# Performance work log

Hardware: AMD Instinct MI355X
Metric: run time of the kernel (lower is better)

The kernel has to match this reference:

```python
import jax, jax.numpy as jnp
import numpy as np

B, N, K, D = 8, 4096, 8, 256
EPS = 1e-8
LN_EPS = 1e-5


def setup_inputs() -> dict:
    key = jax.random.key(0)
    ks = jax.random.split(key, 9)
    lim_s = float(np.sqrt(6.0 / (K + D)))   # xavier_uniform on (K, D) fan dims
    lim_w = float(np.sqrt(6.0 / (D + D)))   # xavier-ish init for square Linear weights
    return {
        "embeddings": jax.random.normal(ks[0], (B, N, D), jnp.float32),
        "slots_mu": jax.random.uniform(ks[1], (1, K, D), jnp.float32, -lim_s, lim_s),
        "slots_logsigma": jax.random.uniform(ks[2], (1, K, D), jnp.float32, -lim_s, lim_s),
        "mixing_coeffs": jnp.full((1, K), 1.0 / K, jnp.float32),
        "Wq": jax.random.uniform(ks[3], (D, D), jnp.float32, -lim_w, lim_w),
        "Wk": jax.random.uniform(ks[4], (D, D), jnp.float32, -lim_w, lim_w),
        "Wv": jax.random.uniform(ks[5], (D, D), jnp.float32, -lim_w, lim_w),
        "ln_scale": jnp.ones((D,), jnp.float32),
        "ln_bias": jnp.zeros((D,), jnp.float32),
        "noise_init": jax.random.normal(ks[6], (B, K, D), jnp.float32),
        "noise_final": jax.random.normal(ks[7], (B, K, D), jnp.float32),
        "num_iterations": 3,
    }


def _layer_norm(x, scale, bias):
    m = jnp.mean(x, axis=-1, keepdims=True)
    v = jnp.mean((x - m) ** 2, axis=-1, keepdims=True)  # biased var, matches torch LayerNorm
    return (x - m) / jnp.sqrt(v + LN_EPS) * scale + bias


def reference(embeddings, slots_mu, slots_logsigma, mixing_coeffs, Wq, Wk, Wv,
              ln_scale, ln_bias, noise_init, noise_final, num_iterations):
    b, n, d = embeddings.shape
    k = slots_mu.shape[1]
    mix = jnp.broadcast_to(mixing_coeffs, (b, k))               # (B,K)
    mu = jnp.broadcast_to(slots_mu, (b, k, d))                  # (B,K,D)
    sigma = jnp.exp(jnp.broadcast_to(slots_logsigma, (b, k, d)))
    slots = mu + sigma * noise_init                             # slots never updated in loop (faithful)

    x = _layer_norm(embeddings, ln_scale, ln_bias)
    keys = x @ Wk.T                                             # (B,N,D)
    values = x @ Wv.T                                           # (B,N,D)

    log_norm_const = jnp.float32(-0.5 * d * np.log(2.0 * np.pi))
    attn = None
    for _ in range(num_iterations):
        queries = slots @ Wq.T                                  # (B,K,D)
        diff = keys[:, :, None, :] - queries[:, None, :, :]     # (B,N,K,D)
        gll = -0.5 * jnp.sum(diff ** 2 / (sigma[:, None] ** 2 + EPS), axis=-1)  # (B,N,K)
        gll = (log_norm_const
               - 0.5 * jnp.sum(jnp.log(jnp.abs(sigma) + EPS), axis=-1)[:, None, :]
               + gll)
        gll = jnp.clip(gll, -10000.0, 10000.0)
        log_attn = jnp.log(mix + EPS)[:, None, :] + gll         # (B,N,K)
        attn = jax.nn.softmax(log_attn, axis=1)                 # softmax over N
        mu = jnp.einsum('bnk,bnd->bkd', attn, values)           # weighted mean
        diff_v = values[:, :, None, :] - mu[:, None, :, :]      # (B,N,K,D)
        sigma = jnp.einsum('bnk,bnkd->bkd', attn, diff_v ** 2)  # weighted variance
        mix = jnp.sum(attn, axis=1) / n

    sigma = jnp.maximum(jnp.abs(sigma), EPS)
    slots_out = mu + sigma * noise_final
    return slots_out, jnp.transpose(attn, (0, 2, 1))            # (B,K,D), (B,K,N)
```

## Files before the change

### kernel.cpp

```cpp
#include <hip/hip_runtime.h>
#include <math.h>


#define Bd 8
#define Nd 4096
#define Kd 8
#define Dd 256
#define Md (Bd*Nd)
#define NITER 3
#define EPSf 1e-8f
#define LNEPS 1e-5f
#define NCH 64
#define LOGNORM -235.24826450039617f

typedef float f32x4 __attribute__((ext_vector_type(4)));
typedef short bf16x8 __attribute__((ext_vector_type(8)));
typedef unsigned short ushort_t;
typedef unsigned short us4 __attribute__((ext_vector_type(4)));

#define KEYS_OFF 0
#define VALS_OFF (Md*Dd)
#define E_OFF    (2*Md*Dd)
#define Q_OFF    (E_OFF + Bd*Kd*Nd)
#define W_OFF    (Q_OFF + Bd*Kd*Dd)
#define CST_OFF  (W_OFF + Bd*Kd*Dd)
#define MSP_OFF  (CST_OFF + 64)
#define SSP_OFF  (MSP_OFF + Bd*Kd*NCH)
#define PMU_OFF  (SSP_OFF + Bd*Kd*NCH)
#define PS2_OFF  (PMU_OFF + Bd*NCH*Kd*Dd)
#define WH_OFF   (PS2_OFF + Bd*NCH*Kd*Dd)
#define WL_OFF   (WH_OFF + 65536)
#define XH_OFF   (WL_OFF + 65536)
#define XL_OFF   (XH_OFF + Md*Dd/2)
#define WS_TOTAL (XL_OFF + Md*Dd/2)

__device__ __forceinline__ ushort_t f2bf(float f) {
    unsigned u = __float_as_uint(f);
    return (ushort_t)((u + 0x7FFFu + ((u >> 16) & 1u)) >> 16);
}
__device__ __forceinline__ float b2f(ushort_t h) {
    return __uint_as_float(((unsigned)h) << 16);
}
__device__ __forceinline__ void gload_lds16(const void* g, void* l) {
    __builtin_amdgcn_global_load_lds(
        (__attribute__((address_space(1))) void*)g,
        (__attribute__((address_space(3))) void*)l, 16, 0, 0);
}

__global__ __launch_bounds__(256) void k_setup(
        const float* __restrict__ emb, const float* __restrict__ lns,
        const float* __restrict__ lnb, const float* __restrict__ Wk,
        const float* __restrict__ Wv, const float* __restrict__ mu0,
        const float* __restrict__ lsig, const float* __restrict__ nz0,
        const float* __restrict__ Wq, ushort_t* __restrict__ xh,
        ushort_t* __restrict__ xl, ushort_t* __restrict__ Wh,
        ushort_t* __restrict__ Wl, float* __restrict__ qout,
        float* __restrict__ w_ws, float* __restrict__ cst_ws) {
    __shared__ float s_s[256];
    __shared__ float red[256];
    const int bx = blockIdx.x;
    if (bx < 1024) {
        const int tid = threadIdx.x, wave = tid >> 6, lane = tid & 63;
        const int row0 = bx * 32;
        const float4 sc = ((const float4*)lns)[lane];
        const float4 bi = ((const float4*)lnb)[lane];
        for (int rr = 0; rr < 8; ++rr) {
            const int r = row0 + wave * 8 + rr;
            const float4 e4 = ((const float4*)(emb + (size_t)r * Dd))[lane];
            float s = e4.x + e4.y + e4.z + e4.w;
            #pragma unroll
            for (int off = 32; off; off >>= 1) s += __shfl_xor(s, off);
            const float m = s * (1.0f / 256.0f);
            const float dx = e4.x - m, dy = e4.y - m, dz = e4.z - m, dw = e4.w - m;
            float ss = dx * dx + dy * dy + dz * dz + dw * dw;
            #pragma unroll
            for (int off = 32; off; off >>= 1) ss += __shfl_xor(ss, off);
            const float rs = 1.0f / sqrtf(ss * (1.0f / 256.0f) + LNEPS);
            float x[4];
            x[0] = dx * rs * sc.x + bi.x;
            x[1] = dy * rs * sc.y + bi.y;
            x[2] = dz * rs * sc.z + bi.z;
            x[3] = dw * rs * sc.w + bi.w;
            us4 h4, l4;
            #pragma unroll
            for (int j = 0; j < 4; ++j) {
                const ushort_t h = f2bf(x[j]);
                h4[j] = h;
                l4[j] = f2bf(x[j] - b2f(h));
            }
            *(us4*)(xh + (size_t)r * Dd + lane * 4) = h4;
            *(us4*)(xl + (size_t)r * Dd + lane * 4) = l4;
        }
    } else if (bx < 1536) {
        const int r = bx - 1024, d = threadIdx.x;
        const float w = (r < 256) ? Wk[(size_t)r * 256 + d]
                                  : Wv[(size_t)(r - 256) * 256 + d];
        const ushort_t h = f2bf(w);
        Wh[(size_t)r * 256 + d] = h;
        Wl[(size_t)r * 256 + d] = f2bf(w - b2f(h));
    } else {
        const int bk = bx - 1536;
        const int k = bk & 7;
        const int d = threadIdx.x;
        const float sg = expf(lsig[k * 256 + d]);
        s_s[d] = mu0[k * 256 + d] + sg * nz0[(size_t)bk * 256 + d];
        w_ws[(size_t)bk * 256 + d] = 1.0f / (sg * sg + EPSf);
        red[d] = logf(fabsf(sg) + EPSf);
        __syncthreads();
        for (int s = 128; s; s >>= 1) {
            if (d < s) red[d] += red[d + s];
            __syncthreads();
        }
        if (d == 0) cst_ws[bk] = LOGNORM - 0.5f * red[0];
        float acc = 0.0f;
        const float4* Wr = (const float4*)(Wq + (size_t)d * 256);
        const float4* sp = (const float4*)s_s;
        #pragma unroll 8
        for (int j = 0; j < 64; ++j) {
            const float4 w4 = Wr[j], s4 = sp[j];
            acc += w4.x * s4.x + w4.y * s4.y + w4.z * s4.z + w4.w * s4.w;
        }
        qout[(size_t)bk * 256 + d] = acc;
    }
}

__global__ __launch_bounds__(256, 2) void k_gemm(
        const ushort_t* __restrict__ xh, const ushort_t* __restrict__ xl,
        const ushort_t* __restrict__ Wh, const ushort_t* __restrict__ Wl,
        float* __restrict__ keys, float* __restrict__ vals) {
    __shared__ ushort_t Ah[128 * 32], Al[128 * 32];
    __shared__ ushort_t Bh[256 * 32], Bl[256 * 32];
    const int bxf = blockIdx.x;
    const int grp = bxf >> 4, o = bxf & 15;
    const int tile = grp * 8 + (o & 7);
    const int cb = o >> 3;
    const int tid = threadIdx.x, lane = tid & 63, wave = tid >> 6;
    const int row0 = tile * 128;
    const int wm = wave >> 1, wn = wave & 1;

    f32x4 acc[4][8];
    #pragma unroll
    for (int a = 0; a < 4; ++a)
        #pragma unroll
        for (int b = 0; b < 8; ++b) acc[a][b] = (f32x4)(0.0f);

    for (int jb = 0; jb < 256; jb += 32) {
        #pragma unroll
        for (int i = 0; i < 2; ++i) {
            const int p = tid + i * 256;
            const int r = p >> 2, gp = p & 3;
            const int g = gp ^ ((r >> 1) & 3);
            const size_t goff = (size_t)(row0 + r) * 256 + jb + g * 8;
            gload_lds16(xh + goff, &Ah[p * 8]);
            gload_lds16(xl + goff, &Al[p * 8]);
        }
        #pragma unroll
        for (int i = 0; i < 4; ++i) {
            const int p = (wave * 4 + i) * 64 + lane;
            const int r = p >> 2, gp = p & 3;
            const int g = gp ^ ((r >> 1) & 3);
            const size_t goff = (size_t)(cb * 256 + r) * 256 + jb + g * 8;
            gload_lds16(Wh + goff, &Bh[p * 8]);
            gload_lds16(Wl + goff, &Bl[p * 8]);
        }
        __syncthreads();

        bf16x8 bhf[8], blf[8];
        #pragma unroll
        for (int ni = 0; ni < 8; ++ni) {
            const int c = wn * 128 + ni * 16 + (lane & 15);
            const int g = lane >> 4;
            const int off = c * 32 + ((g ^ ((c >> 1) & 3)) << 3);
            bhf[ni] = *(const bf16x8*)&Bh[off];
            blf[ni] = *(const bf16x8*)&Bl[off];
        }
        #pragma unroll
        for (int mi = 0; mi < 4; ++mi) {
            const int rr = wm * 64 + mi * 16 + (lane & 15);
            const int g = lane >> 4;
            const int off = rr * 32 + ((g ^ ((rr >> 1) & 3)) << 3);
            const bf16x8 ah = *(const bf16x8*)&Ah[off];
            const bf16x8 al = *(const bf16x8*)&Al[off];
            #pragma unroll
            for (int ni = 0; ni < 8; ++ni) {
                acc[mi][ni] = __builtin_amdgcn_mfma_f32_16x16x32_bf16(ah, bhf[ni], acc[mi][ni], 0, 0, 0);
                acc[mi][ni] = __builtin_amdgcn_mfma_f32_16x16x32_bf16(ah, blf[ni], acc[mi][ni], 0, 0, 0);
                acc[mi][ni] = __builtin_amdgcn_mfma_f32_16x16x32_bf16(al, bhf[ni], acc[mi][ni], 0, 0, 0);
            }
        }
        __syncthreads();
    }
    float* outp = (cb == 0) ? keys : vals;
    #pragma unroll
    for (int mi = 0; mi < 4; ++mi) {
        const int rbase = row0 + wm * 64 + mi * 16 + ((lane >> 4) << 2);
        #pragma unroll
        for (int ni = 0; ni < 8; ++ni) {
            const int col = wn * 128 + ni * 16 + (lane & 15);
            #pragma unroll
            for (int rg = 0; rg < 4; ++rg)
                outp[(size_t)(rbase + rg) * Dd + col] = acc[mi][ni][rg];
        }
    }
}

__global__ __launch_bounds__(512, 4) void k_fuse(
        const float* __restrict__ keys, const float* __restrict__ vals,
        const float* __restrict__ q_ws, const float* __restrict__ w_ws,
        const float* __restrict__ cst_ws, float* __restrict__ e_glob,
        float* __restrict__ msp, float* __restrict__ ssp,
        float* __restrict__ pmu, float* __restrict__ ps2, const int last) {
    __shared__ float buf[16384];
    __shared__ float e_s[8][64];
    const int tid = threadIdx.x, lane = tid & 63, wv = tid >> 6;
    const int b = blockIdx.x >> 6, chunk = blockIdx.x & 63;
    const int n0 = chunk * 64;
    const int wvu = __builtin_amdgcn_readfirstlane(wv);

    const float* kbase = keys + ((size_t)b * Nd + n0) * Dd;
    #pragma unroll
    for (int i = 0; i < 8; ++i) {
        const int p = i * 512 + tid;
        const int row = p >> 6, gp = p & 63;
        const int g = gp ^ row;
        gload_lds16(kbase + (size_t)row * Dd + g * 4, &buf[p * 4]);
    }
    __syncthreads();

    const float4* qk = (const float4*)(q_ws + ((size_t)b * Kd + wvu) * Dd);
    const float4* wk = (const float4*)(w_ws + ((size_t)b * Kd + wvu) * Dd);
    const float* krow = &buf[lane * 256];
    float ax = 0.f, ay = 0.f, az = 0.f, aw = 0.f;
    #pragma unroll 8
    for (int g = 0; g < 64; ++g) {
        const float4 k4 = *(const float4*)&krow[(g ^ lane) * 4];
        const float4 q4 = qk[g];
        const float4 w4 = wk[g];
        float t;
        t = k4.x - q4.x; ax += t * t * w4.x;
        t = k4.y - q4.y; ay += t * t * w4.y;
        t = k4.z - q4.z; az += t * t * w4.z;
        t = k4.w - q4.w; aw += t * t * w4.w;
    }
    float gv = cst_ws[b * Kd + wvu] - 0.5f * ((ax + ay) + (az + aw));
    gv = fminf(fmaxf(gv, -10000.0f), 10000.0f);
    float m = gv;
    #pragma unroll
    for (int off = 32; off; off >>= 1) m = fmaxf(m, __shfl_xor(m, off));
    const float e = expf(gv - m);
    float ssum = e;
    #pragma unroll
    for (int off = 32; off; off >>= 1) ssum += __shfl_xor(ssum, off);
    e_s[wv][lane] = e;
    if (last) e_glob[((size_t)(b * Kd + wvu)) * Nd + n0 + lane] = e;
    if (lane == 0) {
        msp[(b * Kd + wvu) * NCH + chunk] = m;
        ssp[(b * Kd + wvu) * NCH + chunk] = ssum;
    }
    __syncthreads();

    const float* vbase = vals + ((size_t)b * Nd + n0) * Dd;
    #pragma unroll
    for (int i = 0; i < 8; ++i) {
        const int p = i * 512 + tid;
        gload_lds16(vbase + (size_t)p * 4, &buf[p * 4]);
    }
    __syncthreads();

    float4 mu4 = {0.f, 0.f, 0.f, 0.f}, s24 = {0.f, 0.f, 0.f, 0.f};
    #pragma unroll 8
    for (int n = 0; n < 64; ++n) {
        const float4 v = *(const float4*)&buf[n * 256 + lane * 4];
        const float a = e_s[wv][n];
        mu4.x += a * v.x; mu4.y += a * v.y; mu4.z += a * v.z; mu4.w += a * v.w;
        s24.x += a * v.x * v.x; s24.y += a * v.y * v.y;
        s24.z += a * v.z * v.z; s24.w += a * v.w * v.w;
    }
    const size_t o = (((size_t)(b * NCH + chunk)) * Kd + wv) * Dd + lane * 4;
    *(float4*)(pmu + o) = mu4;
    *(float4*)(ps2 + o) = s24;
}

__global__ __launch_bounds__(256) void k_prep(
        const float* __restrict__ msp, const float* __restrict__ ssp,
        const float* __restrict__ pmu, const float* __restrict__ ps2,
        float* __restrict__ w_ws, float* __restrict__ cst_ws,
        const float* __restrict__ nzf, float* __restrict__ slots_out,
        const float* __restrict__ e_glob, float* __restrict__ attn,
        const int last) {
    __shared__ float wS[64];
    __shared__ float aS[64];
    __shared__ float sinv_s;
    __shared__ float4 muP[4][64];
    __shared__ float4 s2P[4][64];
    const int bk = blockIdx.x;
    const int b = bk >> 3, k = bk & 7;
    const int tid = threadIdx.x, lane = tid & 63, grp = tid >> 6;
    if (grp == 0) {
        const float m_c = msp[bk * NCH + lane];
        const float s_c = ssp[bk * NCH + lane];
        float M = m_c;
        #pragma unroll
        for (int off = 32; off; off >>= 1) M = fmaxf(M, __shfl_xor(M, off));
        const float wc = expf(m_c - M);
        float S = wc * s_c;
        #pragma unroll
        for (int off = 32; off; off >>= 1) S += __shfl_xor(S, off);
        wS[lane] = wc;
        aS[lane] = wc / S;
        if (lane == 0) sinv_s = 1.0f / S;
    }
    __syncthreads();
    float4 am = {0.f, 0.f, 0.f, 0.f}, a2 = {0.f, 0.f, 0.f, 0.f};
    #pragma unroll
    for (int i = 0; i < 16; ++i) {
        const int c = grp * 16 + i;
        const float wc = wS[c];
        const size_t o = (((size_t)(b * NCH + c)) * Kd + k) * Dd + lane * 4;
        const float4 pm = *(const float4*)(pmu + o);
        const float4 p2 = *(const float4*)(ps2 + o);
        am.x += wc * pm.x; am.y += wc * pm.y; am.z += wc * pm.z; am.w += wc * pm.w;
        a2.x += wc * p2.x; a2.y += wc * p2.y; a2.z += wc * p2.z; a2.w += wc * p2.w;
    }
    muP[grp][lane] = am;
    s2P[grp][lane] = a2;
    __syncthreads();
    if (grp == 0) {
        const float sinv = sinv_s;
        float4 mu, E2;
        mu.x = (muP[0][lane].x + muP[1][lane].x + muP[2][lane].x + muP[3][lane].x) * sinv;
        mu.y = (muP[0][lane].y + muP[1][lane].y + muP[2][lane].y + muP[3][lane].y) * sinv;
        mu.z = (muP[0][lane].z + muP[1][lane].z + muP[2][lane].z + muP[3][lane].z) * sinv;
        mu.w = (muP[0][lane].w + muP[1][lane].w + muP[2][lane].w + muP[3][lane].w) * sinv;
        E2.x = (s2P[0][lane].x + s2P[1][lane].x + s2P[2][lane].x + s2P[3][lane].x) * sinv;
        E2.y = (s2P[0][lane].y + s2P[1][lane].y + s2P[2][lane].y + s2P[3][lane].y) * sinv;
        E2.z = (s2P[0][lane].z + s2P[1][lane].z + s2P[2][lane].z + s2P[3][lane].z) * sinv;
        E2.w = (s2P[0][lane].w + s2P[1][lane].w + s2P[2][lane].w + s2P[3][lane].w) * sinv;
        float4 sg;
        sg.x = E2.x - mu.x * mu.x; sg.y = E2.y - mu.y * mu.y;
        sg.z = E2.z - mu.z * mu.z; sg.w = E2.w - mu.w * mu.w;
        float4 wout;
        wout.x = 1.0f / (sg.x * sg.x + EPSf); wout.y = 1.0f / (sg.y * sg.y + EPSf);
        wout.z = 1.0f / (sg.z * sg.z + EPSf); wout.w = 1.0f / (sg.w * sg.w + EPSf);
        *(float4*)(w_ws + (size_t)bk * Dd + lane * 4) = wout;
        const float4 nz = *(const float4*)(nzf + (size_t)bk * Dd + lane * 4);
        float4 so;
        so.x = mu.x + fmaxf(fabsf(sg.x), EPSf) * nz.x;
        so.y = mu.y + fmaxf(fabsf(sg.y), EPSf) * nz.y;
        so.z = mu.z + fmaxf(fabsf(sg.z), EPSf) * nz.z;
        so.w = mu.w + fmaxf(fabsf(sg.w), EPSf) * nz.w;
        *(float4*)(slots_out + (size_t)bk * Dd + lane * 4) = so;
        float lsum = logf(fabsf(sg.x) + EPSf) + logf(fabsf(sg.y) + EPSf)
                   + logf(fabsf(sg.z) + EPSf) + logf(fabsf(sg.w) + EPSf);
        #pragma unroll
        for (int off = 32; off; off >>= 1) lsum += __shfl_xor(lsum, off);
        if (lane == 0) cst_ws[bk] = LOGNORM - 0.5f * lsum;
    }
    if (last) {
        const float4* erow = (const float4*)(e_glob + (size_t)bk * Nd);
        float4* arow = (float4*)(attn + (size_t)bk * Nd);
        #pragma unroll
        for (int i = 0; i < 4; ++i) {
            const int idx = tid + i * 256;
            const float4 e4 = erow[idx];
            const float a = aS[idx >> 4];
            float4 o4;
            o4.x = e4.x * a; o4.y = e4.y * a; o4.z = e4.z * a; o4.w = e4.w * a;
            arow[idx] = o4;
        }
    }
}

extern "C" void kernel_launch(void* const* d_in, const int* in_sizes, int n_in,
                              void* d_out, int out_size, void* d_ws, size_t ws_size,
                              hipStream_t stream) {
    const float* emb  = (const float*)d_in[0];
    const float* mu0  = (const float*)d_in[1];
    const float* lsig = (const float*)d_in[2];
    const float* Wq   = (const float*)d_in[4];
    const float* Wk   = (const float*)d_in[5];
    const float* Wv   = (const float*)d_in[6];
    const float* lns  = (const float*)d_in[7];
    const float* lnb  = (const float*)d_in[8];
    const float* nz0  = (const float*)d_in[9];
    const float* nzf  = (const float*)d_in[10];

    float* ws    = (float*)d_ws;
    float* out   = (float*)d_out;
    float* keys  = ws + KEYS_OFF;
    float* vals  = ws + VALS_OFF;
    float* eglob = ws + E_OFF;
    float* qws   = ws + Q_OFF;
    float* wws   = ws + W_OFF;
    float* cstw  = ws + CST_OFF;
    float* msp   = ws + MSP_OFF;
    float* ssp   = ws + SSP_OFF;
    float* pmu   = ws + PMU_OFF;
    float* ps2   = ws + PS2_OFF;
    ushort_t* Whp = (ushort_t*)(ws + WH_OFF);
    ushort_t* Wlp = (ushort_t*)(ws + WL_OFF);
    ushort_t* xhp = (ushort_t*)(ws + XH_OFF);
    ushort_t* xlp = (ushort_t*)(ws + XL_OFF);
    float* attn = out + Bd * Kd * Dd;

    k_setup<<<1600, 256, 0, stream>>>(emb, lns, lnb, Wk, Wv, mu0, lsig, nz0,
                                      Wq, xhp, xlp, Whp, Wlp, qws, wws, cstw);
    k_gemm<<<512, 256, 0, stream>>>(xhp, xlp, Whp, Wlp, keys, vals);
    for (int it = 0; it < NITER; ++it) {
        const int last = (it == NITER - 1);
        k_fuse<<<512, 512, 0, stream>>>(keys, vals, qws, wws, cstw, eglob,
                                        msp, ssp, pmu, ps2, last);
        k_prep<<<64, 256, 0, stream>>>(msp, ssp, pmu, ps2, wws, cstw, nzf,
                                       out, eglob, attn, last);
    }
    (void)in_sizes; (void)n_in; (void)out_size; (void)ws_size;
}
```

Before: 206.0 us.

## Split fuse kernel into 32-row chunks with 256-thread blocks, two slots per wave

Halves the N-chunk per block in the fused E-step/M-step kernel (64 to 32 rows) and uses 256-thread blocks, doubling the grid to 1024 blocks. Each wave now covers two slots, one per 32-lane half, in the log-likelihood phase and accumulates two slots' partial moments in the weighted-sum phase. The reduction kernel is updated to merge 128 chunk partials through a two-wave cross-wave max/sum. The aim is better occupancy and load balance from a larger grid with less LDS per block. The cost is twice as much partial-sum traffic written and then read back in k_prep.

```diff
diff --git a/kernel.cpp b/kernel.cpp
--- a/kernel.cpp
+++ b/kernel.cpp
@@ -10,7 +10,7 @@
 #define NITER 3
 #define EPSf 1e-8f
 #define LNEPS 1e-5f
-#define NCH 64
+#define NCH 128
 #define LOGNORM -235.24826450039617f
 
 typedef float f32x4 __attribute__((ext_vector_type(4)));
@@ -204,36 +204,38 @@
     }
 }
 
-__global__ __launch_bounds__(512, 4) void k_fuse(
+__global__ __launch_bounds__(256, 4) void k_fuse(
         const float* __restrict__ keys, const float* __restrict__ vals,
         const float* __restrict__ q_ws, const float* __restrict__ w_ws,
         const float* __restrict__ cst_ws, float* __restrict__ e_glob,
         float* __restrict__ msp, float* __restrict__ ssp,
         float* __restrict__ pmu, float* __restrict__ ps2, const int last) {
-    __shared__ float buf[16384];
-    __shared__ float e_s[8][64];
+    __shared__ float buf[8192];
+    __shared__ float e_s[8][32];
     const int tid = threadIdx.x, lane = tid & 63, wv = tid >> 6;
-    const int b = blockIdx.x >> 6, chunk = blockIdx.x & 63;
-    const int n0 = chunk * 64;
-    const int wvu = __builtin_amdgcn_readfirstlane(wv);
+    const int b = blockIdx.x >> 7, chunk = blockIdx.x & 127;
+    const int n0 = chunk * 32;
 
     const float* kbase = keys + ((size_t)b * Nd + n0) * Dd;
     #pragma unroll
     for (int i = 0; i < 8; ++i) {
-        const int p = i * 512 + tid;
+        const int p = i * 256 + tid;
         const int row = p >> 6, gp = p & 63;
         const int g = gp ^ row;
         gload_lds16(kbase + (size_t)row * Dd + g * 4, &buf[p * 4]);
     }
     __syncthreads();
 
-    const float4* qk = (const float4*)(q_ws + ((size_t)b * Kd + wvu) * Dd);
-    const float4* wk = (const float4*)(w_ws + ((size_t)b * Kd + wvu) * Dd);
-    const float* krow = &buf[lane * 256];
+    const int half = lane >> 5, nl = lane & 31;
+    const int k = wv + 4 * half;
+    const int bkf = b * Kd + k;
+    const float4* qk = (const float4*)(q_ws + (size_t)bkf * Dd);
+    const float4* wk = (const float4*)(w_ws + (size_t)bkf * Dd);
+    const float* krow = &buf[nl * 256];
     float ax = 0.f, ay = 0.f, az = 0.f, aw = 0.f;
     #pragma unroll 8
     for (int g = 0; g < 64; ++g) {
-        const float4 k4 = *(const float4*)&krow[(g ^ lane) * 4];
+        const float4 k4 = *(const float4*)&krow[((g ^ nl) & 63) * 4];
         const float4 q4 = qk[g];
         const float4 w4 = wk[g];
         float t;
@@ -242,43 +244,52 @@
         t = k4.z - q4.z; az += t * t * w4.z;
         t = k4.w - q4.w; aw += t * t * w4.w;
     }
-    float gv = cst_ws[b * Kd + wvu] - 0.5f * ((ax + ay) + (az + aw));
+    float gv = cst_ws[bkf] - 0.5f * ((ax + ay) + (az + aw));
     gv = fminf(fmaxf(gv, -10000.0f), 10000.0f);
     float m = gv;
     #pragma unroll
-    for (int off = 32; off; off >>= 1) m = fmaxf(m, __shfl_xor(m, off));
+    for (int off = 16; off; off >>= 1) m = fmaxf(m, __shfl_xor(m, off));
     const float e = expf(gv - m);
     float ssum = e;
     #pragma unroll
-    for (int off = 32; off; off >>= 1) ssum += __shfl_xor(ssum, off);
-    e_s[wv][lane] = e;
-    if (last) e_glob[((size_t)(b * Kd + wvu)) * Nd + n0 + lane] = e;
-    if (lane == 0) {
-        msp[(b * Kd + wvu) * NCH + chunk] = m;
-        ssp[(b * Kd + wvu) * NCH + chunk] = ssum;
+    for (int off = 16; off; off >>= 1) ssum += __shfl_xor(ssum, off);
+    e_s[k][nl] = e;
+    if (last) e_glob[(size_t)bkf * Nd + n0 + nl] = e;
+    if (nl == 0) {
+        msp[bkf * NCH + chunk] = m;
+        ssp[bkf * NCH + chunk] = ssum;
     }
     __syncthreads();
 
     const float* vbase = vals + ((size_t)b * Nd + n0) * Dd;
     #pragma unroll
     for (int i = 0; i < 8; ++i) {
-        const int p = i * 512 + tid;
+        const int p = i * 256 + tid;
         gload_lds16(vbase + (size_t)p * 4, &buf[p * 4]);
     }
     __syncthreads();
 
-    float4 mu4 = {0.f, 0.f, 0.f, 0.f}, s24 = {0.f, 0.f, 0.f, 0.f};
+    const int k1 = wv + 4;
+    float4 muA = {0.f,0.f,0.f,0.f}, s2A = {0.f,0.f,0.f,0.f};
+    float4 muB = {0.f,0.f,0.f,0.f}, s2B = {0.f,0.f,0.f,0.f};
     #pragma unroll 8
-    for (int n = 0; n < 64; ++n) {
+    for (int n = 0; n < 32; ++n) {
         const float4 v = *(const float4*)&buf[n * 256 + lane * 4];
-        const float a = e_s[wv][n];
-        mu4.x += a * v.x; mu4.y += a * v.y; mu4.z += a * v.z; mu4.w += a * v.w;
-        s24.x += a * v.x * v.x; s24.y += a * v.y * v.y;
-        s24.z += a * v.z * v.z; s24.w += a * v.w * v.w;
-    }
-    const size_t o = (((size_t)(b * NCH + chunk)) * Kd + wv) * Dd + lane * 4;
-    *(float4*)(pmu + o) = mu4;
-    *(float4*)(ps2 + o) = s24;
+        const float a0 = e_s[wv][n];
+        const float a1 = e_s[k1][n];
+        const float vx2 = v.x * v.x, vy2 = v.y * v.y;
+        const float vz2 = v.z * v.z, vw2 = v.w * v.w;
+        muA.x += a0 * v.x; muA.y += a0 * v.y; muA.z += a0 * v.z; muA.w += a0 * v.w;
+        s2A.x += a0 * vx2; s2A.y += a0 * vy2; s2A.z += a0 * vz2; s2A.w += a0 * vw2;
+        muB.x += a1 * v.x; muB.y += a1 * v.y; muB.z += a1 * v.z; muB.w += a1 * v.w;
+        s2B.x += a1 * vx2; s2B.y += a1 * vy2; s2B.z += a1 * vz2; s2B.w += a1 * vw2;
+    }
+    const size_t o0 = (((size_t)(b * NCH + chunk)) * Kd + wv) * Dd + lane * 4;
+    const size_t o1 = (((size_t)(b * NCH + chunk)) * Kd + k1) * Dd + lane * 4;
+    *(float4*)(pmu + o0) = muA;
+    *(float4*)(ps2 + o0) = s2A;
+    *(float4*)(pmu + o1) = muB;
+    *(float4*)(ps2 + o1) = s2B;
 }
 
 __global__ __launch_bounds__(256) void k_prep(
@@ -288,33 +299,43 @@
         const float* __restrict__ nzf, float* __restrict__ slots_out,
         const float* __restrict__ e_glob, float* __restrict__ attn,
         const int last) {
-    __shared__ float wS[64];
-    __shared__ float aS[64];
+    __shared__ float wS[128];
+    __shared__ float aS[128];
+    __shared__ float wred[2], wsum[2];
     __shared__ float sinv_s;
     __shared__ float4 muP[4][64];
     __shared__ float4 s2P[4][64];
     const int bk = blockIdx.x;
     const int b = bk >> 3, k = bk & 7;
     const int tid = threadIdx.x, lane = tid & 63, grp = tid >> 6;
-    if (grp == 0) {
-        const float m_c = msp[bk * NCH + lane];
-        const float s_c = ssp[bk * NCH + lane];
-        float M = m_c;
-        #pragma unroll
-        for (int off = 32; off; off >>= 1) M = fmaxf(M, __shfl_xor(M, off));
+    float m_c = 0.0f, s_c = 0.0f;
+    if (tid < 128) {
+        m_c = msp[bk * NCH + tid];
+        s_c = ssp[bk * NCH + tid];
+        float mm = m_c;
+        #pragma unroll
+        for (int off = 32; off; off >>= 1) mm = fmaxf(mm, __shfl_xor(mm, off));
+        if (lane == 0) wred[grp] = mm;
+    }
+    __syncthreads();
+    const float M = fmaxf(wred[0], wred[1]);
+    if (tid < 128) {
         const float wc = expf(m_c - M);
-        float S = wc * s_c;
-        #pragma unroll
-        for (int off = 32; off; off >>= 1) S += __shfl_xor(S, off);
-        wS[lane] = wc;
-        aS[lane] = wc / S;
-        if (lane == 0) sinv_s = 1.0f / S;
-    }
+        wS[tid] = wc;
+        float s = wc * s_c;
+        #pragma unroll
+        for (int off = 32; off; off >>= 1) s += __shfl_xor(s, off);
+        if (lane == 0) wsum[grp] = s;
+    }
+    __syncthreads();
+    const float S = wsum[0] + wsum[1];
+    if (tid < 128) aS[tid] = wS[tid] / S;
+    if (tid == 0) sinv_s = 1.0f / S;
     __syncthreads();
     float4 am = {0.f, 0.f, 0.f, 0.f}, a2 = {0.f, 0.f, 0.f, 0.f};
     #pragma unroll
-    for (int i = 0; i < 16; ++i) {
-        const int c = grp * 16 + i;
+    for (int i = 0; i < 32; ++i) {
+        const int c = grp * 32 + i;
         const float wc = wS[c];
         const size_t o = (((size_t)(b * NCH + c)) * Kd + k) * Dd + lane * 4;
         const float4 pm = *(const float4*)(pmu + o);
@@ -363,7 +384,7 @@
         for (int i = 0; i < 4; ++i) {
             const int idx = tid + i * 256;
             const float4 e4 = erow[idx];
-            const float a = aS[idx >> 4];
+            const float a = aS[idx >> 3];
             float4 o4;
             o4.x = e4.x * a; o4.y = e4.y * a; o4.z = e4.z * a; o4.w = e4.w * a;
             arow[idx] = o4;
@@ -408,8 +429,8 @@
     k_gemm<<<512, 256, 0, stream>>>(xhp, xlp, Whp, Wlp, keys, vals);
     for (int it = 0; it < NITER; ++it) {
         const int last = (it == NITER - 1);
-        k_fuse<<<512, 512, 0, stream>>>(keys, vals, qws, wws, cstw, eglob,
-                                        msp, ssp, pmu, ps2, last);
+        k_fuse<<<1024, 256, 0, stream>>>(keys, vals, qws, wws, cstw, eglob,
+                                         msp, ssp, pmu, ps2, last);
         k_prep<<<64, 256, 0, stream>>>(msp, ssp, pmu, ps2, wws, cstw, nzf,
                                        out, eglob, attn, last);
     }
```

After: 239.7 us. 1.16x slower.

## Double k_fuse chunk size to 128 rows with 1024-thread blocks

Applied to the files above, without the earlier changes.

k_fuse now handles 128 sequence rows per block with 16 waves, two waves per slot, and merges their max, sum and weighted moments through shared memory. The number of chunk partials drops from 64 to 32, which halves the partial buffers k_prep has to read and reduce. In exchange each block needs 128KB of LDS and extra barriers, and only 256 blocks are launched, so occupancy and latency hiding may suffer.

```diff
diff --git a/kernel.cpp b/kernel.cpp
--- a/kernel.cpp
+++ b/kernel.cpp
@@ -10,7 +10,7 @@
 #define NITER 3
 #define EPSf 1e-8f
 #define LNEPS 1e-5f
-#define NCH 64
+#define NCH 32
 #define LOGNORM -235.24826450039617f
 
 typedef float f32x4 __attribute__((ext_vector_type(4)));
@@ -204,32 +204,36 @@
     }
 }
 
-__global__ __launch_bounds__(512, 4) void k_fuse(
+__global__ __launch_bounds__(1024, 4) void k_fuse(
         const float* __restrict__ keys, const float* __restrict__ vals,
         const float* __restrict__ q_ws, const float* __restrict__ w_ws,
         const float* __restrict__ cst_ws, float* __restrict__ e_glob,
         float* __restrict__ msp, float* __restrict__ ssp,
         float* __restrict__ pmu, float* __restrict__ ps2, const int last) {
-    __shared__ float buf[16384];
-    __shared__ float e_s[8][64];
+    __shared__ float buf[32768];
+    __shared__ float e_s[8][128];
+    __shared__ float mex[8][2], sex[8][2];
     const int tid = threadIdx.x, lane = tid & 63, wv = tid >> 6;
-    const int b = blockIdx.x >> 6, chunk = blockIdx.x & 63;
-    const int n0 = chunk * 64;
-    const int wvu = __builtin_amdgcn_readfirstlane(wv);
+    const int b = blockIdx.x >> 5, chunk = blockIdx.x & 31;
+    const int n0 = chunk * 128;
+    const int k = __builtin_amdgcn_readfirstlane(wv & 7);
+    const int sub = __builtin_amdgcn_readfirstlane(wv >> 3);
+    const int bkf = b * Kd + k;
 
     const float* kbase = keys + ((size_t)b * Nd + n0) * Dd;
     #pragma unroll
     for (int i = 0; i < 8; ++i) {
-        const int p = i * 512 + tid;
-        const int row = p >> 6, gp = p & 63;
+        const int p = i * 1024 + tid;
+        const int sb = p >> 12, q = p & 4095;
+        const int row = q >> 6, gp = q & 63;
         const int g = gp ^ row;
-        gload_lds16(kbase + (size_t)row * Dd + g * 4, &buf[p * 4]);
-    }
-    __syncthreads();
-
-    const float4* qk = (const float4*)(q_ws + ((size_t)b * Kd + wvu) * Dd);
-    const float4* wk = (const float4*)(w_ws + ((size_t)b * Kd + wvu) * Dd);
-    const float* krow = &buf[lane * 256];
+        gload_lds16(kbase + (size_t)(sb * 64 + row) * Dd + g * 4, &buf[p * 4]);
+    }
+    __syncthreads();
+
+    const float4* qk = (const float4*)(q_ws + (size_t)bkf * Dd);
+    const float4* wk = (const float4*)(w_ws + (size_t)bkf * Dd);
+    const float* krow = &buf[sub * 16384 + lane * 256];
     float ax = 0.f, ay = 0.f, az = 0.f, aw = 0.f;
     #pragma unroll 8
     for (int g = 0; g < 64; ++g) {
@@ -242,27 +246,31 @@
         t = k4.z - q4.z; az += t * t * w4.z;
         t = k4.w - q4.w; aw += t * t * w4.w;
     }
-    float gv = cst_ws[b * Kd + wvu] - 0.5f * ((ax + ay) + (az + aw));
+    float gv = cst_ws[bkf] - 0.5f * ((ax + ay) + (az + aw));
     gv = fminf(fmaxf(gv, -10000.0f), 10000.0f);
     float m = gv;
     #pragma unroll
     for (int off = 32; off; off >>= 1) m = fmaxf(m, __shfl_xor(m, off));
-    const float e = expf(gv - m);
+    if (lane == 0) mex[k][sub] = m;
+    __syncthreads();
+    const float mf = fmaxf(mex[k][0], mex[k][1]);
+    const float e = expf(gv - mf);
     float ssum = e;
     #pragma unroll
     for (int off = 32; off; off >>= 1) ssum += __shfl_xor(ssum, off);
-    e_s[wv][lane] = e;
-    if (last) e_glob[((size_t)(b * Kd + wvu)) * Nd + n0 + lane] = e;
-    if (lane == 0) {
-        msp[(b * Kd + wvu) * NCH + chunk] = m;
-        ssp[(b * Kd + wvu) * NCH + chunk] = ssum;
-    }
-    __syncthreads();
+    e_s[k][sub * 64 + lane] = e;
+    if (last) e_glob[(size_t)bkf * Nd + n0 + sub * 64 + lane] = e;
+    if (lane == 0) sex[k][sub] = ssum;
+    __syncthreads();
+    if (sub == 0 && lane == 0) {
+        msp[bkf * NCH + chunk] = mf;
+        ssp[bkf * NCH + chunk] = sex[k][0] + sex[k][1];
+    }
 
     const float* vbase = vals + ((size_t)b * Nd + n0) * Dd;
     #pragma unroll
     for (int i = 0; i < 8; ++i) {
-        const int p = i * 512 + tid;
+        const int p = i * 1024 + tid;
         gload_lds16(vbase + (size_t)p * 4, &buf[p * 4]);
     }
     __syncthreads();
@@ -270,15 +278,29 @@
     float4 mu4 = {0.f, 0.f, 0.f, 0.f}, s24 = {0.f, 0.f, 0.f, 0.f};
     #pragma unroll 8
     for (int n = 0; n < 64; ++n) {
-        const float4 v = *(const float4*)&buf[n * 256 + lane * 4];
-        const float a = e_s[wv][n];
+        const int r = sub * 64 + n;
+        const float4 v = *(const float4*)&buf[r * 256 + lane * 4];
+        const float a = e_s[k][r];
         mu4.x += a * v.x; mu4.y += a * v.y; mu4.z += a * v.z; mu4.w += a * v.w;
         s24.x += a * v.x * v.x; s24.y += a * v.y * v.y;
         s24.z += a * v.z * v.z; s24.w += a * v.w * v.w;
     }
-    const size_t o = (((size_t)(b * NCH + chunk)) * Kd + wv) * Dd + lane * 4;
-    *(float4*)(pmu + o) = mu4;
-    *(float4*)(ps2 + o) = s24;
+    __syncthreads();
+    if (sub == 1) {
+        float4* scr = (float4*)&buf[k * 1024 + lane * 8];
+        scr[0] = mu4;
+        scr[1] = s24;
+    }
+    __syncthreads();
+    if (sub == 0) {
+        const float4* scr = (const float4*)&buf[k * 1024 + lane * 8];
+        const float4 pm = scr[0], p2 = scr[1];
+        mu4.x += pm.x; mu4.y += pm.y; mu4.z += pm.z; mu4.w += pm.w;
+        s24.x += p2.x; s24.y += p2.y; s24.z += p2.z; s24.w += p2.w;
+        const size_t o = (((size_t)(b * NCH + chunk)) * Kd + k) * Dd + lane * 4;
+        *(float4*)(pmu + o) = mu4;
+        *(float4*)(ps2 + o) = s24;
+    }
 }
 
 __global__ __launch_bounds__(256) void k_prep(
@@ -288,8 +310,8 @@
         const float* __restrict__ nzf, float* __restrict__ slots_out,
         const float* __restrict__ e_glob, float* __restrict__ attn,
         const int last) {
-    __shared__ float wS[64];
-    __shared__ float aS[64];
+    __shared__ float wS[32];
+    __shared__ float aS[32];
     __shared__ float sinv_s;
     __shared__ float4 muP[4][64];
     __shared__ float4 s2P[4][64];
@@ -297,24 +319,27 @@
     const int b = bk >> 3, k = bk & 7;
     const int tid = threadIdx.x, lane = tid & 63, grp = tid >> 6;
     if (grp == 0) {
-        const float m_c = msp[bk * NCH + lane];
-        const float s_c = ssp[bk * NCH + lane];
+        const int c = lane & 31;
+        const float m_c = msp[bk * NCH + c];
+        const float s_c = ssp[bk * NCH + c];
         float M = m_c;
         #pragma unroll
         for (int off = 32; off; off >>= 1) M = fmaxf(M, __shfl_xor(M, off));
         const float wc = expf(m_c - M);
-        float S = wc * s_c;
+        float S = wc * s_c * 0.5f;
         #pragma unroll
         for (int off = 32; off; off >>= 1) S += __shfl_xor(S, off);
-        wS[lane] = wc;
-        aS[lane] = wc / S;
+        if (lane < 32) {
+            wS[lane] = wc;
+            aS[lane] = wc / S;
+        }
         if (lane == 0) sinv_s = 1.0f / S;
     }
     __syncthreads();
     float4 am = {0.f, 0.f, 0.f, 0.f}, a2 = {0.f, 0.f, 0.f, 0.f};
     #pragma unroll
-    for (int i = 0; i < 16; ++i) {
-        const int c = grp * 16 + i;
+    for (int i = 0; i < 8; ++i) {
+        const int c = grp * 8 + i;
         const float wc = wS[c];
         const size_t o = (((size_t)(b * NCH + c)) * Kd + k) * Dd + lane * 4;
         const float4 pm = *(const float4*)(pmu + o);
@@ -363,7 +388,7 @@
         for (int i = 0; i < 4; ++i) {
             const int idx = tid + i * 256;
             const float4 e4 = erow[idx];
-            const float a = aS[idx >> 4];
+            const float a = aS[idx >> 5];
             float4 o4;
             o4.x = e4.x * a; o4.y = e4.y * a; o4.z = e4.z * a; o4.w = e4.w * a;
             arow[idx] = o4;
@@ -408,8 +433,8 @@
     k_gemm<<<512, 256, 0, stream>>>(xhp, xlp, Whp, Wlp, keys, vals);
     for (int it = 0; it < NITER; ++it) {
         const int last = (it == NITER - 1);
-        k_fuse<<<512, 512, 0, stream>>>(keys, vals, qws, wws, cstw, eglob,
-                                        msp, ssp, pmu, ps2, last);
+        k_fuse<<<256, 1024, 0, stream>>>(keys, vals, qws, wws, cstw, eglob,
+                                         msp, ssp, pmu, ps2, last);
         k_prep<<<64, 256, 0, stream>>>(msp, ssp, pmu, ps2, wws, cstw, nzf,
                                        out, eglob, attn, last);
     }
```

Measured after the change: 207.8 us. Within noise of the previous version (+0.9%).
